# Optimization experiments

Hardware: AMD Instinct MI355X
Metric: run time of the kernel (lower is better)

Reference implementation:

```python
import jax, jax.numpy as jnp
import numpy as np
import math

EMBED_DIM = 768
NUM_HEADS = 12
HEAD_DIM = EMBED_DIM // NUM_HEADS
SPARSITY = 0.1


def setup_inputs() -> dict:
    key = jax.random.key(0)
    ks = jax.random.split(key, 5)
    B, N, D = 4, 1024, EMBED_DIM
    s = 1.0 / math.sqrt(D)
    return {
        "x": jax.random.normal(ks[0], (B, N, D), dtype=jnp.float32),
        "W_qkv": jax.random.normal(ks[1], (D, 3 * D), dtype=jnp.float32) * s,
        "b_qkv": jnp.zeros((3 * D,), dtype=jnp.float32),
        "W_out": jax.random.normal(ks[2], (D, D), dtype=jnp.float32) * s,
        "b_out": jnp.zeros((D,), dtype=jnp.float32),
    }


def reference(x, W_qkv, b_qkv, W_out, b_out):
    B, N, D = x.shape
    H, hd = NUM_HEADS, HEAD_DIM
    qkv = x @ W_qkv + b_qkv                      # [B,N,3D]
    qkv = qkv.reshape(B, N, 3, H, hd).transpose(2, 0, 3, 1, 4)  # [3,B,H,N,hd]
    q, k, v = qkv[0], qkv[1], qkv[2]
    attn = jnp.einsum("bhqd,bhkd->bhqk", q, k) * (1.0 / math.sqrt(hd))  # [B,H,N,N]
    kth = int(N * N * SPARSITY)
    if kth > 0:
        # kth smallest value over the flattened per-(b,h) attention matrix
        flat = attn.reshape(B, H, N * N)
        thr = jnp.sort(flat, axis=-1)[..., kth - 1]               # [B,H]
        attn = jnp.where(attn <= thr[:, :, None, None], -1e9, attn)
    attn = jax.nn.softmax(attn, axis=-1)
    out = jnp.einsum("bhqk,bhkd->bhqd", attn, v)                  # [B,H,N,hd]
    out = out.transpose(0, 2, 1, 3).reshape(B, N, D)
    return out @ W_out + b_out
```

## Files before the change

### kernel.cpp

```cpp
#include <hip/hip_runtime.h>
#include <math.h>

#define SEQ 1024
#define DMODEL 768
#define NHEADS 12
#define HDIM 64
#define D3 2304
#define BH 48
#define NTOK 4096
#define KTH 104857u
#define NBIN 4096
#define BIN0 14336

typedef __bf16 bf16x8 __attribute__((ext_vector_type(8)));
typedef float  f32x4  __attribute__((ext_vector_type(4)));

#define SWZ(row, chunk) ((row) * 32 + (((chunk) ^ (((row) >> 1) & 3)) * 8))

__device__ __forceinline__ void gl16(const ushort* g, ushort* l) {
    __builtin_amdgcn_global_load_lds(
        (__attribute__((address_space(1))) void*)(size_t)(g),
        (__attribute__((address_space(3))) void*)(l), 16, 0, 0);
}

__device__ __forceinline__ void split1(float x, ushort& h, ushort& l) {
    unsigned b  = __float_as_uint(x);
    unsigned hb = (b + 0x7FFFu + ((b >> 16) & 1u)) >> 16;
    float hf = __uint_as_float(hb << 16);
    float r  = x - hf;
    unsigned rb = __float_as_uint(r);
    unsigned lb = (rb + 0x7FFFu + ((rb >> 16) & 1u)) >> 16;
    h = (ushort)hb; l = (ushort)lb;
}

__device__ __forceinline__ ushort bf16rne(float x) {
    unsigned b = __float_as_uint(x);
    return (ushort)((b + 0x7FFFu + ((b >> 16) & 1u)) >> 16);
}

__global__ __launch_bounds__(256) void k_prep(
    const float* __restrict__ x, ushort* __restrict__ xh,
    ushort* __restrict__ xl, int n, unsigned* __restrict__ hist,
    const float* __restrict__ Wqkv, ushort* __restrict__ Wqth,
    ushort* __restrict__ Wqtl,
    const float* __restrict__ Wout, ushort* __restrict__ Woth,
    ushort* __restrict__ Wotl) {
    __shared__ float t[64][65];
    int bx = blockIdx.x, tid = threadIdx.x;
    if (bx < 3072) {
        int g = bx * 256 + tid;
        if (g < BH * NBIN) hist[g] = 0u;
        int i = g * 4;
        if (i >= n) return;
        float4 v = *(const float4*)(x + i);
        ushort4 hh, ll;
        split1(v.x, hh.x, ll.x); split1(v.y, hh.y, ll.y);
        split1(v.z, hh.z, ll.z); split1(v.w, hh.w, ll.w);
        *(ushort4*)(xh + i) = hh;
        *(ushort4*)(xl + i) = ll;
        return;
    }
    const float* W; ushort* Wth; ushort* Wtl; int N, n0, k0;
    if (bx < 3504) {
        int b2 = bx - 3072;
        W = Wqkv; Wth = Wqth; Wtl = Wqtl; N = D3;
        n0 = (b2 % 36) * 64; k0 = (b2 / 36) * 64;
    } else {
        int b2 = bx - 3504;
        W = Wout; Wth = Woth; Wtl = Wotl; N = DMODEL;
        n0 = (b2 % 12) * 64; k0 = (b2 / 12) * 64;
    }
    const int K = DMODEL;
    int r = tid >> 4, c = (tid & 15) * 4;
#pragma unroll
    for (int u = 0; u < 4; u++) {
        int rr = r + u * 16;
        float4 v = *(const float4*)(W + (size_t)(k0 + rr) * N + n0 + c);
        t[rr][c] = v.x; t[rr][c + 1] = v.y; t[rr][c + 2] = v.z; t[rr][c + 3] = v.w;
    }
    __syncthreads();
    int nn = tid >> 2, kc = (tid & 3) * 16;
    ushort hb[16] __attribute__((aligned(16)));
    ushort lb[16] __attribute__((aligned(16)));
#pragma unroll
    for (int j = 0; j < 16; j++) split1(t[kc + j][nn], hb[j], lb[j]);
    ushort* dh = Wth + (size_t)(n0 + nn) * K + k0 + kc;
    ushort* dl = Wtl + (size_t)(n0 + nn) * K + k0 + kc;
    *(uint4*)(dh)     = *(uint4*)&hb[0];
    *(uint4*)(dh + 8) = *(uint4*)&hb[8];
    *(uint4*)(dl)     = *(uint4*)&lb[0];
    *(uint4*)(dl + 8) = *(uint4*)&lb[8];
}

#define STAGE_LDS(ko)                                                           \
    gl16(gAh + (ko), &sA[0][wbase]);                                            \
    gl16(gAh2 + (ko), &sA[0][2048 + wbase]);                                    \
    gl16(gAl + (ko), &sA[1][wbase]);                                            \
    gl16(gAl2 + (ko), &sA[1][2048 + wbase]);                                    \
    gl16(gBh + (ko), &sB[0][wbase]);                                            \
    gl16(gBh2 + (ko), &sB[0][2048 + wbase]);                                    \
    gl16(gBl + (ko), &sB[1][wbase]);                                            \
    gl16(gBl2 + (ko), &sB[1][2048 + wbase]);

#define GEMM_CORE_SETUP(Kdim)                                                   \
    __shared__ ushort sA[2][128 * 32];                                          \
    __shared__ ushort sB[2][128 * 32];                                          \
    int tid = threadIdx.x, lane = tid & 63, wave = tid >> 6;                    \
    int wm = (wave >> 1) * 64, wn = (wave & 1) * 64;                            \
    int l15 = lane & 15, q = lane >> 4;                                         \
    int sr = tid >> 2, sc = tid & 3;                                            \
    const int K = (Kdim);                                                       \
    int scs = sc ^ ((sr >> 1) & 3);          \
    const ushort* gAh = Ah + (size_t)(m0 + sr) * K + scs * 8;                   \
    const ushort* gAl = Al + (size_t)(m0 + sr) * K + scs * 8;                   \
    const ushort* gBh = Bh + (size_t)(n0 + sr) * K + scs * 8;                   \
    const ushort* gBl = Bl + (size_t)(n0 + sr) * K + scs * 8;                   \
    const ushort* gAh2 = gAh + (size_t)64 * K;                                  \
    const ushort* gAl2 = gAl + (size_t)64 * K;                                  \
    const ushort* gBh2 = gBh + (size_t)64 * K;                                  \
    const ushort* gBl2 = gBl + (size_t)64 * K;                                  \
    int wbase = wave * 512;              \
    f32x4 acc[4][4] = {};                                                       \
    STAGE_LDS(0)                                                                \
    __syncthreads();                                                            \
    const int NIT = K / 32;                                                     \
    for (int it = 0; it < NIT; ++it) {                                          \
        bf16x8 fah[4], fal[4], fbh[4], fbl[4];                                  \
        _Pragma("unroll")                                                       \
        for (int mt = 0; mt < 4; mt++) {                                        \
            int rr = wm + mt * 16 + l15;                                        \
            fah[mt] = *(const bf16x8*)(&sA[0][SWZ(rr, q)]);                     \
            fal[mt] = *(const bf16x8*)(&sA[1][SWZ(rr, q)]);                     \
        }                                                                       \
        _Pragma("unroll")                                                       \
        for (int nt = 0; nt < 4; nt++) {                                        \
            int rr = wn + nt * 16 + l15;                                        \
            fbh[nt] = *(const bf16x8*)(&sB[0][SWZ(rr, q)]);                     \
            fbl[nt] = *(const bf16x8*)(&sB[1][SWZ(rr, q)]);                     \
        }                                                                       \
        __syncthreads();                 \
        if (it + 1 < NIT) { STAGE_LDS((it + 1) * 32) }                          \
        _Pragma("unroll")                                                       \
        for (int mt = 0; mt < 4; mt++)                                          \
            _Pragma("unroll")                                                   \
            for (int nt = 0; nt < 4; nt++) {                                    \
                acc[mt][nt] = __builtin_amdgcn_mfma_f32_16x16x32_bf16(          \
                    fah[mt], fbh[nt], acc[mt][nt], 0, 0, 0);                    \
                acc[mt][nt] = __builtin_amdgcn_mfma_f32_16x16x32_bf16(          \
                    fah[mt], fbl[nt], acc[mt][nt], 0, 0, 0);                    \
                acc[mt][nt] = __builtin_amdgcn_mfma_f32_16x16x32_bf16(          \
                    fal[mt], fbh[nt], acc[mt][nt], 0, 0, 0);                    \
            }                                                                   \
        __syncthreads();                   \
    }

__global__ __launch_bounds__(256) void k_gemm_out(
    const ushort* __restrict__ Ah, const ushort* __restrict__ Al,
    const ushort* __restrict__ Bh, const ushort* __restrict__ Bl,
    const float* __restrict__ bias, float* __restrict__ C,
    int M, int N, int Kin) {
    int m0 = blockIdx.y * 128, n0 = blockIdx.x * 128;
    GEMM_CORE_SETUP(Kin)
#pragma unroll
    for (int nt = 0; nt < 4; nt++) {
        int col = n0 + wn + nt * 16 + l15;
        float bv = bias[col];
#pragma unroll
        for (int mt = 0; mt < 4; mt++) {
            int rowb = m0 + wm + mt * 16 + q * 4;
#pragma unroll
            for (int r = 0; r < 4; r++)
                C[(size_t)(rowb + r) * N + col] = acc[mt][nt][r] + bv;
        }
    }
}

__global__ __launch_bounds__(256) void k_gemm_qkv(
    const ushort* __restrict__ Ah, const ushort* __restrict__ Al,
    const ushort* __restrict__ Bh, const ushort* __restrict__ Bl,
    const float* __restrict__ bias,
    ushort* __restrict__ Qh, ushort* __restrict__ Ql,
    ushort* __restrict__ Kh, ushort* __restrict__ Kl,
    ushort* __restrict__ Vth) {
    int m0 = blockIdx.y * 128, n0 = blockIdx.x * 128;
    GEMM_CORE_SETUP(DMODEL)
    int region = n0 / 768;
#pragma unroll
    for (int nt = 0; nt < 4; nt++) {
        int col = n0 + wn + nt * 16 + l15;
        float bv = bias[col];
        int cin = col - region * 768;
        int h = cin >> 6, d = cin & 63;
#pragma unroll
        for (int mt = 0; mt < 4; mt++) {
            int rowb = m0 + wm + mt * 16 + q * 4;
            int b = rowb >> 10;
            int s0 = rowb & 1023;
            int bh = b * NHEADS + h;
            if (region == 2) {
                ushort h4[4] __attribute__((aligned(8)));
#pragma unroll
                for (int r = 0; r < 4; r++)
                    h4[r] = bf16rne(acc[mt][nt][r] + bv);
                size_t off = ((size_t)(bh * 64 + d) << 10) + s0;
                *(ushort4*)(Vth + off) = *(ushort4*)h4;
            } else {
                ushort* Ph = region ? Kh : Qh;
                ushort* Pl = region ? Kl : Ql;
                size_t off = ((size_t)((bh << 10) + s0)) * 64 + d;
#pragma unroll
                for (int r = 0; r < 4; r++) {
                    ushort hs, ls;
                    split1(acc[mt][nt][r] + bv, hs, ls);
                    Ph[off + (size_t)r * 64] = hs;
                    Pl[off + (size_t)r * 64] = ls;
                }
            }
        }
    }
}

__global__ __launch_bounds__(256) void k_scores(
    const ushort* __restrict__ Qh, const ushort* __restrict__ Ql,
    const ushort* __restrict__ Kh, const ushort* __restrict__ Kl,
    unsigned* __restrict__ hist) {
    __shared__ unsigned lh[NBIN];
    int orig = blockIdx.x;
    int wid = (orig & 7) * 96 + (orig >> 3);
    int bh = wid >> 4;
    int rem = wid & 15;
    int i0 = (rem >> 1) * 128;
    int j0b = (rem & 1) * 512;
    int tid = threadIdx.x, lane = tid & 63, wave = tid >> 6;
    int l15 = lane & 15, q = lane >> 4;
    int wj = (wave >> 1) * 64, wi = (wave & 1) * 64;
    for (int i = tid; i < NBIN; i += 256) lh[i] = 0u;
    __syncthreads();

    const ushort* qb  = Qh + ((size_t)bh << 16);
    const ushort* qlb = Ql + ((size_t)bh << 16);
    const ushort* kb  = Kh + ((size_t)bh << 16);
    const ushort* klb = Kl + ((size_t)bh << 16);

    bf16x8 fqh[4][2], fql[4][2];
#pragma unroll
    for (int nt = 0; nt < 4; nt++)
#pragma unroll
        for (int kk = 0; kk < 2; kk++) {
            size_t off = (size_t)(i0 + wi + nt * 16 + l15) * 64 + kk * 32 + q * 8;
            fqh[nt][kk] = *(const bf16x8*)(qb + off);
            fql[nt][kk] = *(const bf16x8*)(qlb + off);
        }
    bf16x8 fkh[2][2], fkl[2][2];
    {
        size_t off = (size_t)(j0b + wj + l15) * 64 + q * 8;
        fkh[0][0] = *(const bf16x8*)(kb + off);
        fkl[0][0] = *(const bf16x8*)(klb + off);
        fkh[0][1] = *(const bf16x8*)(kb + off + 32);
        fkl[0][1] = *(const bf16x8*)(klb + off + 32);
    }

#pragma unroll
    for (int s = 0; s < 16; s++) {
        int cur = s & 1;
        if (s + 1 < 16) {
            int s1 = s + 1;
            int jr = j0b + (s1 >> 2) * 128 + wj + (s1 & 3) * 16;
            size_t off = (size_t)(jr + l15) * 64 + q * 8;
            fkh[cur ^ 1][0] = *(const bf16x8*)(kb + off);
            fkl[cur ^ 1][0] = *(const bf16x8*)(klb + off);
            fkh[cur ^ 1][1] = *(const bf16x8*)(kb + off + 32);
            fkl[cur ^ 1][1] = *(const bf16x8*)(klb + off + 32);
        }
        f32x4 acc[4] = {};
#pragma unroll
        for (int kk = 0; kk < 2; kk++)
#pragma unroll
            for (int nt = 0; nt < 4; nt++) {
                acc[nt] = __builtin_amdgcn_mfma_f32_16x16x32_bf16(
                    fkh[cur][kk], fqh[nt][kk], acc[nt], 0, 0, 0);
                acc[nt] = __builtin_amdgcn_mfma_f32_16x16x32_bf16(
                    fkl[cur][kk], fqh[nt][kk], acc[nt], 0, 0, 0);
                acc[nt] = __builtin_amdgcn_mfma_f32_16x16x32_bf16(
                    fkh[cur][kk], fql[nt][kk], acc[nt], 0, 0, 0);
            }
#pragma unroll
        for (int nt = 0; nt < 4; nt++) {
#pragma unroll
            for (int r = 0; r < 4; r++) {
                ushort u = bf16rne(__expf(acc[nt][r] * 0.125f));
                int bin = (int)u - BIN0;
                bin = (bin < 0) ? 0 : ((bin > NBIN - 1) ? NBIN - 1 : bin);
                atomicAdd(&lh[bin], 1u);
            }
        }
    }
    __syncthreads();
    for (int i = tid; i < NBIN; i += 256) {
        unsigned cc = lh[i];
        if (cc) atomicAdd(&hist[bh * NBIN + i], cc);
    }
}

__global__ __launch_bounds__(256) void k_pv(const ushort* __restrict__ Qh,
                                            const ushort* __restrict__ Ql,
                                            const ushort* __restrict__ Kh,
                                            const ushort* __restrict__ Kl,
                                            const ushort* __restrict__ Vth,
                                            const unsigned* __restrict__ hist,
                                            ushort* __restrict__ ctxh,
                                            ushort* __restrict__ ctxl) {
    __shared__ ushort sK[2][2][32 * 64];
    __shared__ ushort sV[2][64 * 32];
    __shared__ ushort pt[4][32 * 40] __attribute__((aligned(16)));
    __shared__ unsigned ps[256];
    __shared__ unsigned thrS;
    int orig = blockIdx.x;
    int wid = (orig & 7) * 48 + (orig >> 3);
    int bh = wid >> 3;
    int i0 = (wid & 7) * 128;
    int b = bh / NHEADS, h = bh % NHEADS;
    int tid = threadIdx.x, lane = tid & 63, wave = tid >> 6;
    int l15 = lane & 15, q = lane >> 4;

    const ushort* qb  = Qh + ((size_t)bh << 16);
    const ushort* qlb = Ql + ((size_t)bh << 16);
    const ushort* kb  = Kh + ((size_t)bh << 16);
    const ushort* klb = Kl + ((size_t)bh << 16);
    const ushort* vh0 = Vth + ((size_t)bh << 16);

    int sr2 = tid >> 3, sc2 = tid & 7;
    const ushort* gK  = kb  + (size_t)sr2 * 64 + ((sc2 ^ (sr2 & 7)) * 8);
    const ushort* gKl = klb + (size_t)sr2 * 64 + ((sc2 ^ (sr2 & 7)) * 8);
    int sr = tid >> 2, sc = tid & 3;
    const ushort* gV = vh0 + (size_t)sr * 1024 + ((sc ^ ((sr >> 1) & 3)) * 8);
    int wbase = wave * 512;

    gl16(gK,  &sK[0][0][wbase]);
    gl16(gKl, &sK[0][1][wbase]);
    gl16(gV,  &sV[0][wbase]);

    const unsigned* hrow = hist + bh * NBIN;
    unsigned psum = 0;
#pragma unroll
    for (int i = 0; i < 16; i++) psum += hrow[tid * 16 + i];
    ps[tid] = psum;
    __syncthreads();
    unsigned pre = 0;
    for (int u = 0; u < 256; u++) {
        unsigned v = ps[u];
        if (u < tid) pre += v;
    }
    if (pre < KTH && pre + psum >= KTH) {
        unsigned run = pre; int d = 15;
#pragma unroll
        for (int i = 0; i < 16; i++) {
            unsigned v = hrow[tid * 16 + i];
            if (run + v >= KTH) { d = i; break; }
            run += v;
        }
        thrS = (unsigned)(BIN0 + tid * 16 + d);
    }
    __syncthreads();
    unsigned t = thrS;

    bf16x8 fqh[2][2], fql[2][2];
#pragma unroll
    for (int ig = 0; ig < 2; ig++)
#pragma unroll
        for (int kk = 0; kk < 2; kk++) {
            size_t off = (size_t)(i0 + wave * 32 + ig * 16 + l15) * 64 + kk * 32 + q * 8;
            fqh[ig][kk] = *(const bf16x8*)(qb + off);
            fql[ig][kk] = *(const bf16x8*)(qlb + off);
        }

    f32x4 accp[2][4] = {};
    f32x4 lacc[2] = {};
    uint4 onesu = {0x3F803F80u, 0x3F803F80u, 0x3F803F80u, 0x3F803F80u};
    bf16x8 ones = *(bf16x8*)&onesu;
    ushort* myP = &pt[wave][0];

    for (int j0 = 0; j0 < SEQ; j0 += 32) {
        int cur = (j0 >> 5) & 1;
        bf16x8 kh[2][2], kl[2][2];
#pragma unroll
        for (int j16 = 0; j16 < 2; j16++) {
            int row = j16 * 16 + l15, rs = row & 7;
#pragma unroll
            for (int kk = 0; kk < 2; kk++) {
                int off = row * 64 + (((kk * 4 + q) ^ rs) * 8);
                kh[j16][kk] = *(const bf16x8*)(&sK[cur][0][off]);
                kl[j16][kk] = *(const bf16x8*)(&sK[cur][1][off]);
            }
        }
        bf16x8 fvh[4];
#pragma unroll
        for (int nt = 0; nt < 4; nt++)
            fvh[nt] = *(const bf16x8*)(&sV[cur][SWZ(nt * 16 + l15, q)]);
        if (j0 + 32 < SEQ) {
            int nxt = cur ^ 1;
            gl16(gK  + (size_t)(j0 + 32) * 64, &sK[nxt][0][wbase]);
            gl16(gKl + (size_t)(j0 + 32) * 64, &sK[nxt][1][wbase]);
            gl16(gV  + (j0 + 32),              &sV[nxt][wbase]);
        }
        bf16x8 pa[2];
#pragma unroll
        for (int ig = 0; ig < 2; ig++) {
#pragma unroll
            for (int j16 = 0; j16 < 2; j16++) {
                f32x4 s = {};
                s = __builtin_amdgcn_mfma_f32_16x16x32_bf16(kh[j16][0], fqh[ig][0], s, 0, 0, 0);
                s = __builtin_amdgcn_mfma_f32_16x16x32_bf16(kl[j16][0], fqh[ig][0], s, 0, 0, 0);
                s = __builtin_amdgcn_mfma_f32_16x16x32_bf16(kh[j16][0], fql[ig][0], s, 0, 0, 0);
                s = __builtin_amdgcn_mfma_f32_16x16x32_bf16(kh[j16][1], fqh[ig][1], s, 0, 0, 0);
                s = __builtin_amdgcn_mfma_f32_16x16x32_bf16(kl[j16][1], fqh[ig][1], s, 0, 0, 0);
                s = __builtin_amdgcn_mfma_f32_16x16x32_bf16(kh[j16][1], fql[ig][1], s, 0, 0, 0);
                unsigned pb[4];
#pragma unroll
                for (int r = 0; r < 4; r++) {
                    unsigned u = bf16rne(__expf(s[r] * 0.125f));
                    pb[r] = (u <= t) ? 0u : u;
                }
                uint2 w;
                w.x = pb[0] | (pb[1] << 16);
                w.y = pb[2] | (pb[3] << 16);
                *(uint2*)(&myP[(ig * 16 + l15) * 40 + j16 * 16 + q * 4]) = w;
            }
            pa[ig] = *(const bf16x8*)(&myP[(ig * 16 + l15) * 40 + q * 8]);
        }
#pragma unroll
        for (int ig = 0; ig < 2; ig++) {
#pragma unroll
            for (int nt = 0; nt < 4; nt++)
                accp[ig][nt] = __builtin_amdgcn_mfma_f32_16x16x32_bf16(
                    pa[ig], fvh[nt], accp[ig][nt], 0, 0, 0);
            lacc[ig] = __builtin_amdgcn_mfma_f32_16x16x32_bf16(
                pa[ig], ones, lacc[ig], 0, 0, 0);
        }
        __syncthreads();
    }
#pragma unroll
    for (int ig = 0; ig < 2; ig++)
#pragma unroll
        for (int r = 0; r < 4; r++) {
            int i = i0 + wave * 32 + ig * 16 + q * 4 + r;
            float l = lacc[ig][r];
#pragma unroll
            for (int nt = 0; nt < 4; nt++) {
                int d = nt * 16 + l15;
                ushort hs, ls;
                split1(accp[ig][nt][r] / l, hs, ls);
                size_t off = ((size_t)(b * SEQ + i)) * DMODEL + h * 64 + d;
                ctxh[off] = hs;
                ctxl[off] = ls;
            }
        }
}

extern "C" void kernel_launch(void* const* d_in, const int* in_sizes, int n_in,
                              void* d_out, int out_size, void* d_ws, size_t ws_size,
                              hipStream_t stream) {
    const float* x    = (const float*)d_in[0];
    const float* Wqkv = (const float*)d_in[1];
    const float* bqkv = (const float*)d_in[2];
    const float* Wout = (const float*)d_in[3];
    const float* bout = (const float*)d_in[4];
    float* out = (float*)d_out;

    char* ws = (char*)d_ws;
    ushort* Qh  = (ushort*)(ws + 0);
    ushort* Ql  = (ushort*)(ws + 6291456);
    ushort* Kh  = (ushort*)(ws + 12582912);
    ushort* Kl  = (ushort*)(ws + 18874368);
    ushort* Vth = (ushort*)(ws + 25165824);
    ushort* ctxh = (ushort*)(ws + 239075328);
    ushort* ctxl = (ushort*)(ws + 245366784);
    unsigned* hist = (unsigned*)(ws + 251658240);
    ushort* xh     = (ushort*)(ws + 37748736);
    ushort* xl     = (ushort*)(ws + 37748736 + 6291456);
    ushort* Wqkvth = (ushort*)(ws + 37748736 + 12582912);
    ushort* Wqkvtl = (ushort*)(ws + 37748736 + 16121856);
    ushort* Woutth = (ushort*)(ws + 57409536);
    ushort* Wouttl = (ushort*)(ws + 58589184);

    k_prep<<<3648, 256, 0, stream>>>(x, xh, xl, NTOK * DMODEL, hist,
                                     Wqkv, Wqkvth, Wqkvtl, Wout, Woutth, Wouttl);
    k_gemm_qkv<<<dim3(D3 / 128, NTOK / 128), 256, 0, stream>>>(
        xh, xl, Wqkvth, Wqkvtl, bqkv, Qh, Ql, Kh, Kl, Vth);
    k_scores<<<768, 256, 0, stream>>>(Qh, Ql, Kh, Kl, hist);
    k_pv<<<384, 256, 0, stream>>>(Qh, Ql, Kh, Kl, Vth, hist, ctxh, ctxl);
    k_gemm_out<<<dim3(DMODEL / 128, NTOK / 128), 256, 0, stream>>>(
        ctxh, ctxl, Woutth, Wouttl, bout, out, NTOK, DMODEL, DMODEL);
}
```

Before: 254.1 us.

## Add XCD-aware block remapping, MFMA priority hints, and wave-shuffle prefix scan

The two GEMMs now use a 1D grid with an XCD-aware remap, so blocks sharing an M slab land on the same XCD and reuse its L2. s_setprio raises wave priority around the MFMA sections in the GEMM core, the scores kernel and the PV kernel, to improve overlap with memory traffic. The serial 256-element prefix sum over histogram partials in k_pv is replaced by a wave shuffle scan plus per-wave totals. These are several independent tweaks, and the remap assumes fixed grid sizes.

```diff
diff --git a/kernel.cpp b/kernel.cpp
--- a/kernel.cpp
+++ b/kernel.cpp
@@ -140,6 +140,7 @@
         }                                                                       \
         __syncthreads();                 \
         if (it + 1 < NIT) { STAGE_LDS((it + 1) * 32) }                          \
+        __builtin_amdgcn_s_setprio(1);                                          \
         _Pragma("unroll")                                                       \
         for (int mt = 0; mt < 4; mt++)                                          \
             _Pragma("unroll")                                                   \
@@ -151,6 +152,7 @@
                 acc[mt][nt] = __builtin_amdgcn_mfma_f32_16x16x32_bf16(          \
                     fal[mt], fbh[nt], acc[mt][nt], 0, 0, 0);                    \
             }                                                                   \
+        __builtin_amdgcn_s_setprio(0);                                          \
         __syncthreads();                   \
     }
 
@@ -159,7 +161,12 @@
     const ushort* __restrict__ Bh, const ushort* __restrict__ Bl,
     const float* __restrict__ bias, float* __restrict__ C,
     int M, int N, int Kin) {
-    int m0 = blockIdx.y * 128, n0 = blockIdx.x * 128;
+    int orig = blockIdx.x;
+    int xcd = orig & 7, local = orig >> 3;
+    int mslab = xcd >> 1, nhalf = xcd & 1;
+    int ml = local / 3, nl = local % 3;
+    int m0 = (mslab * 8 + ml) * 128;
+    int n0 = (nhalf * 3 + nl) * 128;
     GEMM_CORE_SETUP(Kin)
 #pragma unroll
     for (int nt = 0; nt < 4; nt++) {
@@ -182,7 +189,12 @@
     ushort* __restrict__ Qh, ushort* __restrict__ Ql,
     ushort* __restrict__ Kh, ushort* __restrict__ Kl,
     ushort* __restrict__ Vth) {
-    int m0 = blockIdx.y * 128, n0 = blockIdx.x * 128;
+    int orig = blockIdx.x;
+    int xcd = orig & 7, local = orig >> 3;
+    int mslab = xcd >> 1, nhalf = xcd & 1;
+    int ml = local / 9, nl = local % 9;
+    int m0 = (mslab * 8 + ml) * 128;
+    int n0 = (nhalf * 9 + nl) * 128;
     GEMM_CORE_SETUP(DMODEL)
     int region = n0 / 768;
 #pragma unroll
@@ -273,6 +285,7 @@
             fkl[cur ^ 1][1] = *(const bf16x8*)(klb + off + 32);
         }
         f32x4 acc[4] = {};
+        __builtin_amdgcn_s_setprio(1);
 #pragma unroll
         for (int kk = 0; kk < 2; kk++)
 #pragma unroll
@@ -284,6 +297,7 @@
                 acc[nt] = __builtin_amdgcn_mfma_f32_16x16x32_bf16(
                     fkh[cur][kk], fql[nt][kk], acc[nt], 0, 0, 0);
             }
+        __builtin_amdgcn_s_setprio(0);
 #pragma unroll
         for (int nt = 0; nt < 4; nt++) {
 #pragma unroll
@@ -313,7 +327,7 @@
     __shared__ ushort sK[2][2][32 * 64];
     __shared__ ushort sV[2][64 * 32];
     __shared__ ushort pt[4][32 * 40] __attribute__((aligned(16)));
-    __shared__ unsigned ps[256];
+    __shared__ unsigned wtot[4];
     __shared__ unsigned thrS;
     int orig = blockIdx.x;
     int wid = (orig & 7) * 48 + (orig >> 3);
@@ -344,13 +358,19 @@
     unsigned psum = 0;
 #pragma unroll
     for (int i = 0; i < 16; i++) psum += hrow[tid * 16 + i];
-    ps[tid] = psum;
+    unsigned incl = psum;
+#pragma unroll
+    for (int off = 1; off < 64; off <<= 1) {
+        unsigned xx = __shfl_up(incl, off, 64);
+        if (lane >= off) incl += xx;
+    }
+    if (lane == 63) wtot[wave] = incl;
     __syncthreads();
-    unsigned pre = 0;
-    for (int u = 0; u < 256; u++) {
-        unsigned v = ps[u];
-        if (u < tid) pre += v;
-    }
+    unsigned base = 0;
+#pragma unroll
+    for (int w2 = 0; w2 < 4; w2++)
+        if (w2 < wave) base += wtot[w2];
+    unsigned pre = base + incl - psum;
     if (pre < KTH && pre + psum >= KTH) {
         unsigned run = pre; int d = 15;
 #pragma unroll
@@ -403,6 +423,7 @@
             gl16(gKl + (size_t)(j0 + 32) * 64, &sK[nxt][1][wbase]);
             gl16(gV  + (j0 + 32),              &sV[nxt][wbase]);
         }
+        __builtin_amdgcn_s_setprio(1);
         bf16x8 pa[2];
 #pragma unroll
         for (int ig = 0; ig < 2; ig++) {
@@ -437,6 +458,7 @@
             lacc[ig] = __builtin_amdgcn_mfma_f32_16x16x32_bf16(
                 pa[ig], ones, lacc[ig], 0, 0, 0);
         }
+        __builtin_amdgcn_s_setprio(0);
         __syncthreads();
     }
 #pragma unroll
@@ -485,10 +507,10 @@
 
     k_prep<<<3648, 256, 0, stream>>>(x, xh, xl, NTOK * DMODEL, hist,
                                      Wqkv, Wqkvth, Wqkvtl, Wout, Woutth, Wouttl);
-    k_gemm_qkv<<<dim3(D3 / 128, NTOK / 128), 256, 0, stream>>>(
+    k_gemm_qkv<<<576, 256, 0, stream>>>(
         xh, xl, Wqkvth, Wqkvtl, bqkv, Qh, Ql, Kh, Kl, Vth);
     k_scores<<<768, 256, 0, stream>>>(Qh, Ql, Kh, Kl, hist);
     k_pv<<<384, 256, 0, stream>>>(Qh, Ql, Kh, Kl, Vth, hist, ctxh, ctxl);
-    k_gemm_out<<<dim3(DMODEL / 128, NTOK / 128), 256, 0, stream>>>(
+    k_gemm_out<<<192, 256, 0, stream>>>(
         ctxh, ctxl, Woutth, Wouttl, bout, out, NTOK, DMODEL, DMODEL);
 }
```

Result: faster. 237.1 us (-6.7%).
